# Kernel optimization log

Measured on AMD Instinct MI355X. Metric: run time of the kernel, lower is better.

The kernel has to match this reference:

```python
import jax, jax.numpy as jnp
import numpy as np


def _conv(x, k, pad):
    # x: [B,1,H,W], k: [1,1,kh,kw]
    return jax.lax.conv_general_dilated(
        x, k, window_strides=(1, 1), padding=[(pad, pad), (pad, pad)],
        dimension_numbers=('NCHW', 'OIHW', 'NCHW'))


def _gauss_kernel(size=15, sigma=2.0):
    c = np.arange(size, dtype=np.float32) - size // 2
    k = np.exp(-(c[:, None] ** 2 + c[None, :] ** 2) / (2.0 * sigma ** 2))
    k = k / k.sum()
    return jnp.asarray(k, dtype=jnp.float32)[None, None]


_SOBEL_X = jnp.array([[[[-1., 0., 1.], [-2., 0., 2.], [-1., 0., 1.]]]], dtype=jnp.float32)
_SOBEL_Y = jnp.array([[[[-1., -2., -1.], [0., 0., 0.], [1., 2., 1.]]]], dtype=jnp.float32)
_GAUSS = _gauss_kernel(15, 2.0)


def _edge_density(img):
    gray = 0.299 * img[:, 0] + 0.587 * img[:, 1] + 0.114 * img[:, 2]  # [B,H,W]
    box = jnp.ones((1, 1, 5, 5), jnp.float32) / 25.0  # avg_pool2d, count_include_pad
    blurred = _conv(gray[:, None], box, 2)
    gx = _conv(blurred, _SOBEL_X, 1)
    gy = _conv(blurred, _SOBEL_Y, 1)
    mag = jnp.sqrt(gx ** 2 + gy ** 2)
    hi = mag.max() * 0.2
    lo = hi * 0.3
    edge_map = ((mag > lo) & (mag < hi)).astype(jnp.float32)
    return _conv(edge_map, _GAUSS, 7)  # [B,1,H,W]


def _color_sparsity(img):
    # Replaces the O(K*B*H*W) python loop over unique quantized colors with a
    # 32^3-bin histogram (scatter-add) and a single per-pixel gather.
    b, c, h, w = img.shape
    idx = jnp.clip(jnp.round(img * 31.0), 0, 31).astype(jnp.int32)  # [B,3,H,W]
    code = idx[:, 0] * 1024 + idx[:, 1] * 32 + idx[:, 2]  # [B,H,W]
    counts = jnp.zeros(32 * 32 * 32, jnp.float32).at[code.reshape(-1)].add(1.0)
    prob = counts[code] / float(b * h * w)  # [B,H,W]
    return (-jnp.log(prob + 1e-9) * 1.5)[:, None]  # [B,1,H,W]


def setup_inputs() -> dict:
    key = jax.random.key(0)
    img = jax.random.uniform(key, (1, 3, 3072, 3072), dtype=jnp.float32)
    return {
        'img': img,
        'alpha': jnp.asarray(0.5, dtype=jnp.float32),
        'beta': jnp.asarray(0.5, dtype=jnp.float32),
    }


def reference(img, alpha, beta):
    ed = _edge_density(img)
    cs = _color_sparsity(img)
    en = (ed - ed.min()) / (ed.max() - ed.min() + 1e-9)
    cn = (cs - cs.min()) / (cs.max() - cs.min() + 1e-9)
    return jax.nn.sigmoid(alpha * en + beta * cn)  # [B,1,H,W]
```

## Files before the change

### kernel.cpp

```cpp
#include <hip/hip_runtime.h>
#include <math.h>

#define TW 3072
#define TH 3072
#define NPIX (TW*TH)

__device__ __forceinline__ int qcode(float r, float g, float b) {
    int ir = min(max((int)rintf(__fmul_rn(r, 31.f)), 0), 31);
    int ig = min(max((int)rintf(__fmul_rn(g, 31.f)), 0), 31);
    int ib = min(max((int)rintf(__fmul_rn(b, 31.f)), 0), 31);
    return ir * 1024 + ig * 32 + ib;
}

__device__ __forceinline__ float grayf(float r, float g, float b) {
    return __fadd_rn(__fadd_rn(__fmul_rn(0.299f, r), __fmul_rn(0.587f, g)),
                     __fmul_rn(0.114f, b));
}

__global__ __launch_bounds__(1024) void k_pre(const float4* __restrict__ img4,
                                              float4* __restrict__ gray4,
                                              ushort4* __restrict__ code4,
                                              unsigned* __restrict__ parthist,
                                              unsigned* __restrict__ scal) {
    if (blockIdx.x == 0 && threadIdx.x == 0) {
        scal[0] = 0u;
        scal[1] = 0x7F800000u;
        scal[2] = 0u;
        scal[3] = 0u;
        scal[4] = 0xFFFFFFFFu;
    }
    __shared__ unsigned lh[16384];
    for (int t = threadIdx.x; t < 16384; t += 1024) lh[t] = 0u;
    __syncthreads();
    const int total4 = NPIX / 4;
    const int stride = 256 * 1024;
    int base = blockIdx.x * 1024 + threadIdx.x;
    float4 rn = img4[base], gn = img4[base + total4], bn = img4[base + 2 * total4];
#pragma unroll
    for (int k = 0; k < 9; k++) {
        int p = base + k * stride;
        float4 r = rn, g = gn, b = bn;
        if (k < 8) {
            int pn = p + stride;
            rn = img4[pn]; gn = img4[pn + total4]; bn = img4[pn + 2 * total4];
        }
        float4 gy;
        gy.x = grayf(r.x, g.x, b.x); gy.y = grayf(r.y, g.y, b.y);
        gy.z = grayf(r.z, g.z, b.z); gy.w = grayf(r.w, g.w, b.w);
        gray4[p] = gy;
        int c0 = qcode(r.x, g.x, b.x), c1 = qcode(r.y, g.y, b.y);
        int c2 = qcode(r.z, g.z, b.z), c3 = qcode(r.w, g.w, b.w);
        atomicAdd(&lh[c0 >> 1], (c0 & 1) ? 0x10000u : 1u);
        atomicAdd(&lh[c1 >> 1], (c1 & 1) ? 0x10000u : 1u);
        atomicAdd(&lh[c2 >> 1], (c2 & 1) ? 0x10000u : 1u);
        atomicAdd(&lh[c3 >> 1], (c3 & 1) ? 0x10000u : 1u);
        ushort4 cc;
        cc.x = (unsigned short)c0; cc.y = (unsigned short)c1;
        cc.z = (unsigned short)c2; cc.w = (unsigned short)c3;
        code4[p] = cc;
    }
    __syncthreads();
    unsigned* dst = parthist + (size_t)blockIdx.x * 16384;
    for (int t = threadIdx.x; t < 16384; t += 1024) dst[t] = lh[t];
}

__global__ __launch_bounds__(1024) void k_reduce(const unsigned* __restrict__ parthist,
                                                 float* __restrict__ cstab,
                                                 unsigned* __restrict__ scal) {
    __shared__ unsigned slo[1024], shi[1024];
    int tid = threadIdx.x;
    int tsub = tid >> 6;
    int pl = tid & 63;
    int b = blockIdx.x * 64 + pl;
    unsigned lo = 0u, hi = 0u;
#pragma unroll
    for (int j = 0; j < 16; j++) {
        unsigned v = parthist[(size_t)(tsub * 16 + j) * 16384 + b];
        lo += v & 0xFFFFu;
        hi += v >> 16;
    }
    slo[tid] = lo;
    shi[tid] = hi;
    __syncthreads();
    if (tid < 64) {
        unsigned Lo = 0u, Hi = 0u;
#pragma unroll
        for (int t = 0; t < 16; t++) { Lo += slo[t * 64 + tid]; Hi += shi[t * 64 + tid]; }
        const float N = (float)NPIX;
        int bb = blockIdx.x * 64 + tid;
        cstab[2 * bb]     = -logf((float)Lo / N + 1e-9f) * 1.5f;
        cstab[2 * bb + 1] = -logf((float)Hi / N + 1e-9f) * 1.5f;
        unsigned mx = max(Lo, Hi);
        unsigned mn = 0xFFFFFFFFu;
        if (Lo) mn = Lo;
        if (Hi) mn = min(mn, Hi);
#pragma unroll
        for (int o = 32; o > 0; o >>= 1) {
            mx = max(mx, (unsigned)__shfl_down((int)mx, o));
            mn = min(mn, (unsigned)__shfl_down((int)mn, o));
        }
        if (tid == 0) { atomicMax(&scal[3], mx); atomicMin(&scal[4], mn); }
    }
}

__device__ __forceinline__ void blockMaxMinAtomic(float vmax, float vmin,
                                                  unsigned* pmax, unsigned* pmin) {
#pragma unroll
    for (int o = 32; o > 0; o >>= 1) {
        vmax = fmaxf(vmax, __shfl_down(vmax, o));
        vmin = fminf(vmin, __shfl_down(vmin, o));
    }
    __shared__ float smax[8], smin[8];
    int lane = threadIdx.x & 63, wv = threadIdx.x >> 6;
    if (lane == 0) { smax[wv] = vmax; smin[wv] = vmin; }
    __syncthreads();
    if (threadIdx.x == 0) {
        int nw = blockDim.x >> 6;
        float a = smax[0], b = smin[0];
        for (int k = 1; k < nw; k++) { a = fmaxf(a, smax[k]); b = fminf(b, smin[k]); }
        if (pmax) atomicMax(pmax, __float_as_uint(a));
        if (pmin) atomicMin(pmin, __float_as_uint(b));
    }
}

#define BS_W 256
#define BS_H 24
#define GTW 264
#define GTH 30
#define BLW 260
#define BLH 26
__global__ __launch_bounds__(512) void k_boxsobel(const float* __restrict__ g,
                                                  float* __restrict__ mag,
                                                  unsigned* __restrict__ scal) {
    __shared__ float GT[GTH * GTW];
    __shared__ float BL[BLH * BLW];
    int tid = threadIdx.x;
    int x0 = blockIdx.x * BS_W;
    int y0 = blockIdx.y * BS_H;
    {
        float tmp[16];
#pragma unroll
        for (int u = 0; u < 16; u++) {
            int t = tid + u * 512;
            int ly = t / GTW, lx = t - ly * GTW;
            int y = y0 - 3 + ly, x = x0 - 3 + lx;
            bool in = (t < GTH * GTW) && ((unsigned)y < TH) && ((unsigned)x < TW);
            tmp[u] = in ? g[(size_t)y * TW + x] : 0.f;
        }
#pragma unroll
        for (int u = 0; u < 16; u++) {
            int t = tid + u * 512;
            if (t < GTH * GTW) GT[t] = tmp[u];
        }
    }
    __syncthreads();
    for (int t = tid; t < BLH * 65; t += 512) {
        int by = t / 65, gx = t - by * 65;
        int c0 = gx * 4;
        float acc[4] = {0.f, 0.f, 0.f, 0.f};
#pragma unroll
        for (int a = 0; a < 5; a++) {
            const float* rp = &GT[(by + a) * GTW + c0];
            float4 A = *(const float4*)rp;
            float4 B = *(const float4*)(rp + 4);
            float v[8] = {A.x, A.y, A.z, A.w, B.x, B.y, B.z, B.w};
#pragma unroll
            for (int j = 0; j < 4; j++)
#pragma unroll
                for (int b = 0; b < 5; b++)
                    acc[j] = __fadd_rn(acc[j], __fmul_rn(v[j + b], 0.04f));
        }
        int yb = y0 - 1 + by;
        float4 o;
        float* ov = (float*)&o;
#pragma unroll
        for (int j = 0; j < 4; j++) {
            int xb = x0 - 1 + c0 + j;
            ov[j] = ((unsigned)yb < TH && (unsigned)xb < TW) ? acc[j] : 0.f;
        }
        *(float4*)&BL[by * BLW + c0] = o;
    }
    __syncthreads();
    float tmax = 0.f;
    for (int t = tid; t < BS_H * 64; t += 512) {
        int oy = t >> 6, gx = t & 63;
        int c0 = gx * 4;
        float v[3][6];
#pragma unroll
        for (int a = 0; a < 3; a++) {
            const float* rp = &BL[(oy + a) * BLW + c0];
            float4 P = *(const float4*)rp;
            float2 Q = *(const float2*)(rp + 4);
            v[a][0] = P.x; v[a][1] = P.y; v[a][2] = P.z; v[a][3] = P.w;
            v[a][4] = Q.x; v[a][5] = Q.y;
        }
        float4 mo;
        float* mv = (float*)&mo;
#pragma unroll
        for (int j = 0; j < 4; j++) {
            float gxv = 0.f;
            gxv = __fadd_rn(gxv, __fmul_rn(-1.f, v[0][j + 0]));
            gxv = __fadd_rn(gxv, v[0][j + 2]);
            gxv = __fadd_rn(gxv, __fmul_rn(-2.f, v[1][j + 0]));
            gxv = __fadd_rn(gxv, __fmul_rn(2.f, v[1][j + 2]));
            gxv = __fadd_rn(gxv, __fmul_rn(-1.f, v[2][j + 0]));
            gxv = __fadd_rn(gxv, v[2][j + 2]);
            float gyv = 0.f;
            gyv = __fadd_rn(gyv, __fmul_rn(-1.f, v[0][j + 0]));
            gyv = __fadd_rn(gyv, __fmul_rn(-2.f, v[0][j + 1]));
            gyv = __fadd_rn(gyv, __fmul_rn(-1.f, v[0][j + 2]));
            gyv = __fadd_rn(gyv, v[2][j + 0]);
            gyv = __fadd_rn(gyv, __fmul_rn(2.f, v[2][j + 1]));
            gyv = __fadd_rn(gyv, v[2][j + 2]);
            float m = sqrtf(__fadd_rn(__fmul_rn(gxv, gxv), __fmul_rn(gyv, gyv)));
            mv[j] = m;
            tmax = fmaxf(tmax, m);
        }
        *(float4*)&mag[(size_t)(y0 + oy) * TW + x0 + c0] = mo;
    }
    blockMaxMinAtomic(tmax, 0.f, &scal[0], nullptr);
}

#define GS_W 256
#define GS_H 48
#define E_H 62
#define EWB 10
__global__ __launch_bounds__(512) void k_gauss(const float* __restrict__ mag,
                                               float* __restrict__ ed,
                                               const unsigned* __restrict__ scal,
                                               unsigned* __restrict__ scalw) {
    __shared__ float wt[15];
    __shared__ unsigned E8[E_H * EWB];
    __shared__ float EH[E_H * GS_W];
    if (threadIdx.x == 0) {
        float w[15];
        float s = 0.f;
        for (int t = 0; t < 15; t++) {
            int c = t - 7;
            w[t] = expf(-(float)(c * c) * 0.125f);
            s += w[t];
        }
        for (int t = 0; t < 15; t++) wt[t] = w[t] / s;
    }
    __syncthreads();
    float magmax = __uint_as_float(scal[0]);
    float hi = __fmul_rn(magmax, 0.2f);
    float lo = __fmul_rn(hi, 0.3f);
    int tid = threadIdx.x;
    int lane = tid & 63, wave = tid >> 6;
    int x0 = blockIdx.x * GS_W;
    int y0 = blockIdx.y * GS_H;
    for (int item0 = wave * 5; item0 < E_H * 5; item0 += 40) {
        float mv5[5];
#pragma unroll
        for (int u = 0; u < 5; u++) {
            int item = item0 + u;
            int ly = item / 5, ch = item - ly * 5;
            int y = y0 - 7 + ly;
            int lx = ch * 64 + lane;
            int x = x0 - 7 + lx;
            mv5[u] = ((unsigned)y < TH && lx < 270 && (unsigned)x < TW)
                         ? mag[(size_t)y * TW + x] : 0.f;
        }
#pragma unroll
        for (int u = 0; u < 5; u++) {
            int item = item0 + u;
            int ly = item / 5, ch = item - ly * 5;
            unsigned long long mask = __ballot(mv5[u] > lo && mv5[u] < hi);
            if (lane < 2) E8[ly * EWB + ch * 2 + lane] = (unsigned)(mask >> (32 * lane));
        }
    }
    __syncthreads();
    for (int t = tid; t < E_H * 64; t += 512) {
        int ly = t >> 6, gx = t & 63;
        int c0 = gx * 4;
        int w0 = c0 >> 5, sh = c0 & 31;
        unsigned lo32 = E8[ly * EWB + w0];
        unsigned hi32 = E8[ly * EWB + w0 + 1];
        unsigned long long win = (((unsigned long long)hi32 << 32) | lo32) >> sh;
        float e[18];
#pragma unroll
        for (int j = 0; j < 18; j++) e[j] = (float)((unsigned)(win >> j) & 1u);
        float4 o;
        float* ov = (float*)&o;
#pragma unroll
        for (int j = 0; j < 4; j++) {
            float acc = 0.f;
#pragma unroll
            for (int k = 0; k < 15; k++) acc = fmaf(e[j + k], wt[k], acc);
            ov[j] = acc;
        }
        *(float4*)&EH[ly * GS_W + c0] = o;
    }
    __syncthreads();
    float tmin = INFINITY, tmax = 0.f;
    {
        int c0 = lane * 4;
        int r0 = wave * 6;
        float acc[6][4];
#pragma unroll
        for (int s = 0; s < 6; s++) {
            acc[s][0] = 0.f; acc[s][1] = 0.f; acc[s][2] = 0.f; acc[s][3] = 0.f;
        }
#pragma unroll
        for (int j = 0; j < 20; j++) {
            float4 v = *(const float4*)&EH[(r0 + j) * GS_W + c0];
#pragma unroll
            for (int s = 0; s < 6; s++) {
                int k = j - s;
                if (k >= 0 && k < 15) {
                    acc[s][0] = fmaf(v.x, wt[k], acc[s][0]);
                    acc[s][1] = fmaf(v.y, wt[k], acc[s][1]);
                    acc[s][2] = fmaf(v.z, wt[k], acc[s][2]);
                    acc[s][3] = fmaf(v.w, wt[k], acc[s][3]);
                }
            }
        }
#pragma unroll
        for (int s = 0; s < 6; s++) {
            float4 o;
            o.x = acc[s][0]; o.y = acc[s][1]; o.z = acc[s][2]; o.w = acc[s][3];
            *(float4*)&ed[(size_t)(y0 + r0 + s) * TW + x0 + c0] = o;
            tmin = fminf(tmin, fminf(fminf(o.x, o.y), fminf(o.z, o.w)));
            tmax = fmaxf(tmax, fmaxf(fmaxf(o.x, o.y), fmaxf(o.z, o.w)));
        }
    }
    blockMaxMinAtomic(tmax, tmin, &scalw[2], &scalw[1]);
}

__global__ __launch_bounds__(1024) void k_final(float4* __restrict__ io4,
                                                const ushort4* __restrict__ code4,
                                                const float* __restrict__ cstab,
                                                const unsigned* __restrict__ scal,
                                                const float* __restrict__ alphap,
                                                const float* __restrict__ betap) {
    __shared__ unsigned short cnS[32768];
    const float N = (float)NPIX;
    float csmin = -logf((float)scal[3] / N + 1e-9f) * 1.5f;
    float csmax = -logf((float)scal[4] / N + 1e-9f) * 1.5f;
    float csrange = csmax - csmin + 1e-9f;
    for (int t = threadIdx.x; t < 32768; t += 1024) {
        float cn = (cstab[t] - csmin) / csrange;
        int q = (int)rintf(cn * 65535.f);
        cnS[t] = (unsigned short)min(max(q, 0), 65535);
    }
    float edmin = __uint_as_float(scal[1]);
    float edmax = __uint_as_float(scal[2]);
    float edrange = edmax - edmin + 1e-9f;
    float alpha = *alphap, beta = *betap;
    __syncthreads();
    const int total4 = NPIX / 4;
    int stride = gridDim.x * blockDim.x;
    for (int p = blockIdx.x * blockDim.x + threadIdx.x; p < total4; p += stride) {
        float4 edv4 = io4[p];
        ushort4 cc = code4[p];
        float edv[4] = {edv4.x, edv4.y, edv4.z, edv4.w};
        unsigned short cv[4] = {cc.x, cc.y, cc.z, cc.w};
        float ov[4];
#pragma unroll
        for (int t = 0; t < 4; t++) {
            float en = (edv[t] - edmin) / edrange;
            float cn = (float)cnS[cv[t]] * (1.f / 65535.f);
            float x = alpha * en + beta * cn;
            ov[t] = 1.f / (1.f + expf(-x));
        }
        float4 o;
        o.x = ov[0]; o.y = ov[1]; o.z = ov[2]; o.w = ov[3];
        io4[p] = o;
    }
}

extern "C" void kernel_launch(void* const* d_in, const int* in_sizes, int n_in,
                              void* d_out, int out_size, void* d_ws, size_t ws_size,
                              hipStream_t stream) {
    const float* img = (const float*)d_in[0];
    const float* alphap = (const float*)d_in[1];
    const float* betap = (const float*)d_in[2];
    float* out = (float*)d_out;

    char* ws = (char*)d_ws;
    unsigned* scal = (unsigned*)ws;
    float* cstab = (float*)(ws + 1024 + 131072);
    float* G = (float*)(ws + 524288);
    float* M = (float*)(ws + 524288 + (size_t)NPIX * 4);
    unsigned short* code = (unsigned short*)(ws + 524288 + (size_t)NPIX * 8);
    unsigned* parthist = (unsigned*)M;

    hipLaunchKernelGGL(k_pre, dim3(256), dim3(1024), 0, stream,
                       (const float4*)img, (float4*)G, (ushort4*)code, parthist, scal);
    hipLaunchKernelGGL(k_reduce, dim3(256), dim3(1024), 0, stream, parthist, cstab, scal);
    hipLaunchKernelGGL(k_boxsobel, dim3(TW / BS_W, TH / BS_H), dim3(512), 0, stream,
                       G, M, scal);
    hipLaunchKernelGGL(k_gauss, dim3(TW / GS_W, TH / GS_H), dim3(512), 0, stream,
                       M, out, scal, scal);
    hipLaunchKernelGGL(k_final, dim3(512), dim3(1024), 0, stream, (float4*)out,
                       (const ushort4*)code, cstab, scal, alphap, betap);
}
```

Measured before the change: 291.1 us.

## Fold histogram reduction into box-sobel launch and restructure final pass

The separate histogram-reduce kernel is removed. Its work now runs in 256 extra blocks appended to the box/sobel grid, so it overlaps with the convolution and one launch disappears. The partial histograms move to their own workspace region so they no longer alias the magnitude buffer that the box/sobel blocks write. The final kernel builds its quantized colour table with vectorized float4 loads and packed 32-bit shared stores. It also issues its two pixel loads before the barrier and uses exactly 1152 blocks, so no grid-stride loop remains. This relies on NPIX/8 being divisible by 1024 and on enough workspace for the relocated buffer.

```diff
diff --git a/kernel.cpp b/kernel.cpp
--- a/kernel.cpp
+++ b/kernel.cpp
@@ -64,45 +64,6 @@
     for (int t = threadIdx.x; t < 16384; t += 1024) dst[t] = lh[t];
 }
 
-__global__ __launch_bounds__(1024) void k_reduce(const unsigned* __restrict__ parthist,
-                                                 float* __restrict__ cstab,
-                                                 unsigned* __restrict__ scal) {
-    __shared__ unsigned slo[1024], shi[1024];
-    int tid = threadIdx.x;
-    int tsub = tid >> 6;
-    int pl = tid & 63;
-    int b = blockIdx.x * 64 + pl;
-    unsigned lo = 0u, hi = 0u;
-#pragma unroll
-    for (int j = 0; j < 16; j++) {
-        unsigned v = parthist[(size_t)(tsub * 16 + j) * 16384 + b];
-        lo += v & 0xFFFFu;
-        hi += v >> 16;
-    }
-    slo[tid] = lo;
-    shi[tid] = hi;
-    __syncthreads();
-    if (tid < 64) {
-        unsigned Lo = 0u, Hi = 0u;
-#pragma unroll
-        for (int t = 0; t < 16; t++) { Lo += slo[t * 64 + tid]; Hi += shi[t * 64 + tid]; }
-        const float N = (float)NPIX;
-        int bb = blockIdx.x * 64 + tid;
-        cstab[2 * bb]     = -logf((float)Lo / N + 1e-9f) * 1.5f;
-        cstab[2 * bb + 1] = -logf((float)Hi / N + 1e-9f) * 1.5f;
-        unsigned mx = max(Lo, Hi);
-        unsigned mn = 0xFFFFFFFFu;
-        if (Lo) mn = Lo;
-        if (Hi) mn = min(mn, Hi);
-#pragma unroll
-        for (int o = 32; o > 0; o >>= 1) {
-            mx = max(mx, (unsigned)__shfl_down((int)mx, o));
-            mn = min(mn, (unsigned)__shfl_down((int)mn, o));
-        }
-        if (tid == 0) { atomicMax(&scal[3], mx); atomicMin(&scal[4], mn); }
-    }
-}
-
 __device__ __forceinline__ void blockMaxMinAtomic(float vmax, float vmin,
                                                   unsigned* pmax, unsigned* pmin) {
 #pragma unroll
@@ -129,14 +90,59 @@
 #define GTH 30
 #define BLW 260
 #define BLH 26
+#define NCONV ((TW/BS_W)*(TH/BS_H))
 __global__ __launch_bounds__(512) void k_boxsobel(const float* __restrict__ g,
                                                   float* __restrict__ mag,
-                                                  unsigned* __restrict__ scal) {
-    __shared__ float GT[GTH * GTW];
-    __shared__ float BL[BLH * BLW];
+                                                  unsigned* __restrict__ scal,
+                                                  const unsigned* __restrict__ parthist,
+                                                  float* __restrict__ cstab) {
+    __shared__ float smem[GTH * GTW + BLH * BLW];
     int tid = threadIdx.x;
-    int x0 = blockIdx.x * BS_W;
-    int y0 = blockIdx.y * BS_H;
+    int bid = blockIdx.x;
+
+    if (bid >= NCONV) {
+        unsigned* slo = (unsigned*)smem;
+        unsigned* shi = slo + 512;
+        int rbid = bid - NCONV;
+        int tsub = tid >> 6;
+        int pl = tid & 63;
+        int b = rbid * 64 + pl;
+        unsigned lo = 0u, hi = 0u;
+#pragma unroll 8
+        for (int j = 0; j < 32; j++) {
+            unsigned v = parthist[(size_t)(tsub * 32 + j) * 16384 + b];
+            lo += v & 0xFFFFu;
+            hi += v >> 16;
+        }
+        slo[tid] = lo;
+        shi[tid] = hi;
+        __syncthreads();
+        if (tid < 64) {
+            unsigned Lo = 0u, Hi = 0u;
+#pragma unroll
+            for (int t = 0; t < 8; t++) { Lo += slo[t * 64 + tid]; Hi += shi[t * 64 + tid]; }
+            const float N = (float)NPIX;
+            int bb = rbid * 64 + tid;
+            cstab[2 * bb]     = -logf((float)Lo / N + 1e-9f) * 1.5f;
+            cstab[2 * bb + 1] = -logf((float)Hi / N + 1e-9f) * 1.5f;
+            unsigned mx = max(Lo, Hi);
+            unsigned mn = 0xFFFFFFFFu;
+            if (Lo) mn = Lo;
+            if (Hi) mn = min(mn, Hi);
+#pragma unroll
+            for (int o = 32; o > 0; o >>= 1) {
+                mx = max(mx, (unsigned)__shfl_down((int)mx, o));
+                mn = min(mn, (unsigned)__shfl_down((int)mn, o));
+            }
+            if (tid == 0) { atomicMax(&scal[3], mx); atomicMin(&scal[4], mn); }
+        }
+        return;
+    }
+
+    float* GT = smem;
+    float* BL = smem + GTH * GTW;
+    int x0 = (bid % (TW / BS_W)) * BS_W;
+    int y0 = (bid / (TW / BS_W)) * BS_H;
     {
         float tmp[16];
 #pragma unroll
@@ -339,23 +345,40 @@
     float csmin = -logf((float)scal[3] / N + 1e-9f) * 1.5f;
     float csmax = -logf((float)scal[4] / N + 1e-9f) * 1.5f;
     float csrange = csmax - csmin + 1e-9f;
-    for (int t = threadIdx.x; t < 32768; t += 1024) {
-        float cn = (cstab[t] - csmin) / csrange;
-        int q = (int)rintf(cn * 65535.f);
-        cnS[t] = (unsigned short)min(max(q, 0), 65535);
+    {
+        float4 cv[8];
+#pragma unroll
+        for (int u = 0; u < 8; u++)
+            cv[u] = ((const float4*)cstab)[threadIdx.x + u * 1024];
+        unsigned* cnS32 = (unsigned*)cnS;
+#pragma unroll
+        for (int u = 0; u < 8; u++) {
+            int t4 = threadIdx.x + u * 1024;
+            float vv[4] = {cv[u].x, cv[u].y, cv[u].z, cv[u].w};
+            unsigned q[4];
+#pragma unroll
+            for (int j = 0; j < 4; j++) {
+                float cn = (vv[j] - csmin) / csrange;
+                int qi = (int)rintf(cn * 65535.f);
+                q[j] = (unsigned)min(max(qi, 0), 65535);
+            }
+            cnS32[2 * t4]     = q[0] | (q[1] << 16);
+            cnS32[2 * t4 + 1] = q[2] | (q[3] << 16);
+        }
     }
     float edmin = __uint_as_float(scal[1]);
     float edmax = __uint_as_float(scal[2]);
     float edrange = edmax - edmin + 1e-9f;
     float alpha = *alphap, beta = *betap;
-    __syncthreads();
-    const int total4 = NPIX / 4;
-    int stride = gridDim.x * blockDim.x;
-    for (int p = blockIdx.x * blockDim.x + threadIdx.x; p < total4; p += stride) {
-        float4 edv4 = io4[p];
-        ushort4 cc = code4[p];
-        float edv[4] = {edv4.x, edv4.y, edv4.z, edv4.w};
-        unsigned short cv[4] = {cc.x, cc.y, cc.z, cc.w};
+    const int half = NPIX / 8;
+    int p0 = blockIdx.x * 1024 + threadIdx.x;
+    int p1 = p0 + half;
+    float4 e0 = io4[p0]; ushort4 cc0 = code4[p0];
+    float4 e1 = io4[p1]; ushort4 cc1 = code4[p1];
+    __syncthreads();
+    {
+        float edv[4] = {e0.x, e0.y, e0.z, e0.w};
+        unsigned short cv[4] = {cc0.x, cc0.y, cc0.z, cc0.w};
         float ov[4];
 #pragma unroll
         for (int t = 0; t < 4; t++) {
@@ -364,9 +387,22 @@
             float x = alpha * en + beta * cn;
             ov[t] = 1.f / (1.f + expf(-x));
         }
-        float4 o;
-        o.x = ov[0]; o.y = ov[1]; o.z = ov[2]; o.w = ov[3];
-        io4[p] = o;
+        float4 o; o.x = ov[0]; o.y = ov[1]; o.z = ov[2]; o.w = ov[3];
+        io4[p0] = o;
+    }
+    {
+        float edv[4] = {e1.x, e1.y, e1.z, e1.w};
+        unsigned short cv[4] = {cc1.x, cc1.y, cc1.z, cc1.w};
+        float ov[4];
+#pragma unroll
+        for (int t = 0; t < 4; t++) {
+            float en = (edv[t] - edmin) / edrange;
+            float cn = (float)cnS[cv[t]] * (1.f / 65535.f);
+            float x = alpha * en + beta * cn;
+            ov[t] = 1.f / (1.f + expf(-x));
+        }
+        float4 o; o.x = ov[0]; o.y = ov[1]; o.z = ov[2]; o.w = ov[3];
+        io4[p1] = o;
     }
 }
 
@@ -385,14 +421,14 @@
     float* M = (float*)(ws + 524288 + (size_t)NPIX * 4);
     unsigned short* code = (unsigned short*)(ws + 524288 + (size_t)NPIX * 8);
     unsigned* parthist = (unsigned*)M;
+    parthist = (unsigned*)(ws + 524288 + (size_t)NPIX * 10);
 
     hipLaunchKernelGGL(k_pre, dim3(256), dim3(1024), 0, stream,
                        (const float4*)img, (float4*)G, (ushort4*)code, parthist, scal);
-    hipLaunchKernelGGL(k_reduce, dim3(256), dim3(1024), 0, stream, parthist, cstab, scal);
-    hipLaunchKernelGGL(k_boxsobel, dim3(TW / BS_W, TH / BS_H), dim3(512), 0, stream,
-                       G, M, scal);
+    hipLaunchKernelGGL(k_boxsobel, dim3(NCONV + 256), dim3(512), 0, stream,
+                       G, M, scal, parthist, cstab);
     hipLaunchKernelGGL(k_gauss, dim3(TW / GS_W, TH / GS_H), dim3(512), 0, stream,
                        M, out, scal, scal);
-    hipLaunchKernelGGL(k_final, dim3(512), dim3(1024), 0, stream, (float4*)out,
+    hipLaunchKernelGGL(k_final, dim3(1152), dim3(1024), 0, stream, (float4*)out,
                        (const ushort4*)code, cstab, scal, alphap, betap);
 }
```

Result: no change. 296.5 us (+1.8%).
